# Kernel optimization log

Measured on AMD Instinct MI355X. Metric: run time of the kernel, lower is better.

The kernel has to match this reference:

```python
import jax, jax.numpy as jnp
import numpy as np

# Coarse-to-fine lossless 3D segmentation (Seg3dLossless), batch=1, C=1.
RES = [17, 33, 65, 129]          # odd resolutions, stride (RF-1)/(R-1) is integral
RF = RES[-1]
B_MIN, B_MAX = -1.0, 1.0
BAL = 0.5                        # balance_value
N_CONFLICT_ITERS = 2             # fixed unroll of the data-dependent while-loop


def _mlp(pts, w1, b1, w2, b2, w3, b3):
    # query_func: occupancy MLP on normalized (x,y,z) points -> [N]
    h = jax.nn.relu(pts @ w1 + b1)
    h = jax.nn.relu(h @ w2 + b2)
    return jax.nn.sigmoid(h @ w3 + b3)[..., 0]


def _eval_grid(R, w1, b1, w2, b2, w3, b3):
    # batch_eval with align_corners=False: coords2D = (coord + 0.5)/RF, mapped to [B_MIN,B_MAX]
    s = (RF - 1) // (R - 1)
    c = jnp.arange(R, dtype=jnp.float32) * s                 # final-res integer coords
    p = (c + 0.5) / RF * (B_MAX - B_MIN) + B_MIN
    zz, yy, xx = jnp.meshgrid(p, p, p, indexing='ij')        # [D,H,W]
    pts = jnp.stack([xx, yy, zz], axis=-1).reshape(-1, 3)    # (x,y,z) order
    return _mlp(pts, w1, b1, w2, b2, w3, b3).reshape(R, R, R)


def _resize(x, R):
    # trilinear, align_corners=True: out index j -> in coord j*(in-1)/(out-1)
    c = jnp.linspace(0.0, x.shape[0] - 1.0, R)
    zz, yy, xx = jnp.meshgrid(c, c, c, indexing='ij')
    return jax.scipy.ndimage.map_coordinates(x, [zz, yy, xx], order=1, mode='nearest')


def _dilate(m):
    # smooth_conv3x3 (mean filter) followed by >0 == 3x3x3 binary dilation
    f = jax.lax.reduce_window(m.astype(jnp.float32), 0.0, jax.lax.max,
                              (3, 3, 3), (1, 1, 1), 'SAME')
    return f > 0.0


def setup_inputs() -> dict:
    key = jax.random.key(0)
    k1, k2, k3 = jax.random.split(key, 3)
    H = 64
    return {
        'w1': jax.random.normal(k1, (3, H), jnp.float32) * 0.8,
        'b1': jnp.zeros((H,), jnp.float32),
        'w2': jax.random.normal(k2, (H, H), jnp.float32) * (1.0 / np.sqrt(H)),
        'b2': jnp.zeros((H,), jnp.float32),
        'w3': jax.random.normal(k3, (H, 1), jnp.float32) * (1.0 / np.sqrt(H)),
        'b3': jnp.zeros((1,), jnp.float32),
    }


def reference(w1, b1, w2, b2, w3, b3):
    params = (w1, b1, w2, b2, w3, b3)
    # level 0: dense eval on the coarse grid
    occ = _eval_grid(RES[0], *params)                        # [R0,R0,R0]
    s0 = (RF - 1) // (RES[0] - 1)
    calculated = jnp.zeros((RF, RF, RF), bool).at[::s0, ::s0, ::s0].set(True)

    for R in RES[1:]:
        s = (RF - 1) // (R - 1)
        valid = _resize((occ > BAL).astype(jnp.float32), R)  # no-grad mask path
        occ_i = _resize(occ, R)                              # differentiable interp
        boundary = _dilate((valid > 0.0) & (valid < 1.0))
        calc_l = calculated[::s, ::s, ::s]
        boundary = boundary & (~calc_l)                      # skip already-evaluated voxels
        occ_true = _eval_grid(R, *params)                    # query_func at this level
        occ = jnp.where(boundary, occ_true, occ_i)           # scatter of occupancys_topk
        calc_l = calc_l | boundary
        # conflict resolution: re-query 3^3 neighbors of sign-flip voxels
        conflict = boundary & ((occ_i - BAL) * (occ_true - BAL) < 0.0)
        for _ in range(N_CONFLICT_ITERS):
            nbr = _dilate(conflict) & (~calc_l)
            occ_prev = occ
            occ = jnp.where(nbr, occ_true, occ)
            calc_l = calc_l | nbr
            conflict = nbr & ((occ_prev - BAL) * (occ_true - BAL) < 0.0)
        calculated = calculated.at[::s, ::s, ::s].set(calc_l)

    return occ[None, None]                                   # (1, 1, D, H, W)
```

## Files before the change

kernel.cpp:

```cpp
#include <hip/hip_runtime.h>

#define HH 64

static __global__ void k_set_ones(unsigned char* __restrict__ p, int n){
  int i = blockIdx.x * blockDim.x + threadIdx.x;
  if (i < n) p[i] = 1;
}

static __global__ void k_eval_mlp(
    const float* __restrict__ w1, const float* __restrict__ b1,
    const float* __restrict__ w2, const float* __restrict__ b2,
    const float* __restrict__ w3, const float* __restrict__ b3,
    float* __restrict__ out, int R, int s)
{
  __shared__ float sw1[3*HH];
  __shared__ float sb1[HH];
  __shared__ float sw2t[HH*HH];
  __shared__ float sb2[HH];
  __shared__ float sw3[HH];
  __shared__ float sb3s[1];
  const int t = threadIdx.x;
  for (int idx = t; idx < HH*HH; idx += 256){
    int j = idx >> 6, i = idx & 63;
    sw2t[idx] = w2[i*HH + j];
  }
  if (t < 3*HH) sw1[t] = w1[t];
  if (t < HH){ sb1[t] = b1[t]; sb2[t] = b2[t]; sw3[t] = w3[t]; }
  if (t == 0) sb3s[0] = b3[0];
  __syncthreads();

  const unsigned int n = (unsigned int)R * (unsigned int)R * (unsigned int)R;
  const int lane = t & 63;
  const int half = lane >> 5;
  const int ibase = half * 32;
  const unsigned int gwave = (blockIdx.x * 256u + (unsigned int)t) >> 6;
  const unsigned int pid = gwave * 32u + (unsigned int)(lane & 31);
  if (pid >= n) return;

  const unsigned int c = pid % (unsigned int)R;
  const unsigned int r = pid / (unsigned int)R;
  const unsigned int b = r % (unsigned int)R;
  const unsigned int a = r / (unsigned int)R;
  const float inv129x2 = 2.0f / 129.0f;
  const float x = ((float)(c * (unsigned int)s) + 0.5f) * inv129x2 - 1.0f;
  const float y = ((float)(b * (unsigned int)s) + 0.5f) * inv129x2 - 1.0f;
  const float z = ((float)(a * (unsigned int)s) + 0.5f) * inv129x2 - 1.0f;

  float h1[32];
  #pragma unroll
  for (int k = 0; k < 32; ++k){
    int i = ibase + k;
    float v = sb1[i];
    v = fmaf(x, sw1[i],        v);
    v = fmaf(y, sw1[HH + i],   v);
    v = fmaf(z, sw1[2*HH + i], v);
    h1[k] = fmaxf(v, 0.0f);
  }
  float o = sb3s[0];
  #pragma unroll 4
  for (int j = 0; j < HH; ++j){
    const float* wr = &sw2t[j*HH + ibase];
    float acc = 0.0f;
    #pragma unroll
    for (int k = 0; k < 32; ++k) acc = fmaf(h1[k], wr[k], acc);
    acc += __shfl_xor(acc, 32);
    o = fmaf(fmaxf(acc + sb2[j], 0.0f), sw3[j], o);
  }
  if (half == 0) out[pid] = 1.0f / (1.0f + expf(-o));
}

static __global__ void k_eval_sparse(
    const float* __restrict__ w1, const float* __restrict__ b1,
    const float* __restrict__ w2, const float* __restrict__ b2,
    const float* __restrict__ w3, const float* __restrict__ b3,
    const int* __restrict__ idxl, const unsigned int* __restrict__ cnt,
    const float* __restrict__ occ_i,
    float* __restrict__ out, unsigned char* __restrict__ mism,
    int R, int s)
{
  if (blockIdx.x * 128u >= *cnt) return;
  __shared__ float sw1[3*HH];
  __shared__ float sb1[HH];
  __shared__ float sw2t[HH*HH];
  __shared__ float sb2[HH];
  __shared__ float sw3[HH];
  __shared__ float sb3s[1];
  const int t = threadIdx.x;
  for (int idx = t; idx < HH*HH; idx += 256){
    int j = idx >> 6, i = idx & 63;
    sw2t[idx] = w2[i*HH + j];
  }
  if (t < 3*HH) sw1[t] = w1[t];
  if (t < HH){ sb1[t] = b1[t]; sb2[t] = b2[t]; sw3[t] = w3[t]; }
  if (t == 0) sb3s[0] = b3[0];
  __syncthreads();

  const unsigned int count = *cnt;
  const int lane = t & 63;
  const int half = lane >> 5;
  const int ibase = half * 32;
  const unsigned int gwave = (blockIdx.x * 256u + (unsigned int)t) >> 6;
  const unsigned int slot = gwave * 32u + (unsigned int)(lane & 31);
  if (slot >= count) return;
  const unsigned int pid = (unsigned int)idxl[slot];

  const unsigned int c = pid % (unsigned int)R;
  const unsigned int r = pid / (unsigned int)R;
  const unsigned int b = r % (unsigned int)R;
  const unsigned int a = r / (unsigned int)R;
  const float inv129x2 = 2.0f / 129.0f;
  const float x = ((float)(c * (unsigned int)s) + 0.5f) * inv129x2 - 1.0f;
  const float y = ((float)(b * (unsigned int)s) + 0.5f) * inv129x2 - 1.0f;
  const float z = ((float)(a * (unsigned int)s) + 0.5f) * inv129x2 - 1.0f;

  float h1[32];
  #pragma unroll
  for (int k = 0; k < 32; ++k){
    int i = ibase + k;
    float v = sb1[i];
    v = fmaf(x, sw1[i],        v);
    v = fmaf(y, sw1[HH + i],   v);
    v = fmaf(z, sw1[2*HH + i], v);
    h1[k] = fmaxf(v, 0.0f);
  }
  float o = sb3s[0];
  #pragma unroll 4
  for (int j = 0; j < HH; ++j){
    const float* wr = &sw2t[j*HH + ibase];
    float acc = 0.0f;
    #pragma unroll
    for (int k = 0; k < 32; ++k) acc = fmaf(h1[k], wr[k], acc);
    acc += __shfl_xor(acc, 32);
    o = fmaf(fmaxf(acc + sb2[j], 0.0f), sw3[j], o);
  }
  if (half == 0){
    float ot = 1.0f / (1.0f + expf(-o));
    out[pid] = ot;
    mism[pid] = ((occ_i[pid] - 0.5f) * (ot - 0.5f) < 0.0f) ? (unsigned char)1 : (unsigned char)0;
  }
}

static __global__ __launch_bounds__(256) void k_resize_b0(
    const float* __restrict__ prev,
    const unsigned char* __restrict__ calc_prev,
    float* __restrict__ occ_i,
    unsigned char* __restrict__ bnd0,
    unsigned char* __restrict__ calc_out,
    int R, int Rp)
{
  const unsigned int n = (unsigned int)R * (unsigned int)R * (unsigned int)R;
  unsigned int gid = blockIdx.x * 256u + threadIdx.x;
  if (gid >= n) return;
  int c = (int)(gid % (unsigned int)R);
  unsigned int r = gid / (unsigned int)R;
  int b = (int)(r % (unsigned int)R);
  int a = (int)(r / (unsigned int)R);
  int a0 = a >> 1, da = a & 1;
  int b0i = b >> 1, db = b & 1;
  int c0 = c >> 1, dc = c & 1;
  float sum = 0.0f;
  int cnt = 0;
  const int tot = (da + 1) * (db + 1) * (dc + 1);
  for (int dz = 0; dz <= da; ++dz)
    for (int dy = 0; dy <= db; ++dy)
      for (int dx = 0; dx <= dc; ++dx){
        float v = prev[((unsigned int)(a0 + dz) * (unsigned int)Rp + (unsigned int)(b0i + dy)) * (unsigned int)Rp + (unsigned int)(c0 + dx)];
        sum += v;
        cnt += (v > 0.5f) ? 1 : 0;
      }
  occ_i[gid] = sum / (float)tot;
  bnd0[gid] = (cnt > 0 && cnt < tot) ? 1 : 0;
  calc_out[gid] = ((da | db | dc) == 0)
      ? calc_prev[((unsigned int)a0 * (unsigned int)Rp + (unsigned int)b0i) * (unsigned int)Rp + (unsigned int)c0]
      : (unsigned char)0;
}

static __global__ __launch_bounds__(256) void k_resize_boundary(
    const float* __restrict__ prev, const float* __restrict__ occ_true,
    const unsigned char* __restrict__ calc_prev,
    float* __restrict__ occ_i, unsigned char* __restrict__ bnd0,
    unsigned char* __restrict__ mism, unsigned char* __restrict__ calc_out,
    int R, int Rp)
{
  const unsigned int n = (unsigned int)R * (unsigned int)R * (unsigned int)R;
  unsigned int gid = blockIdx.x * 256u + threadIdx.x;
  if (gid >= n) return;
  int c = (int)(gid % (unsigned int)R);
  unsigned int r = gid / (unsigned int)R;
  int b = (int)(r % (unsigned int)R);
  int a = (int)(r / (unsigned int)R);
  int a0 = a >> 1, da = a & 1;
  int b0i = b >> 1, db = b & 1;
  int c0 = c >> 1, dc = c & 1;
  float sum = 0.0f;
  int cnt = 0;
  const int tot = (da + 1) * (db + 1) * (dc + 1);
  for (int dz = 0; dz <= da; ++dz)
    for (int dy = 0; dy <= db; ++dy)
      for (int dx = 0; dx <= dc; ++dx){
        float v = prev[((unsigned int)(a0 + dz) * (unsigned int)Rp + (unsigned int)(b0i + dy)) * (unsigned int)Rp + (unsigned int)(c0 + dx)];
        sum += v;
        cnt += (v > 0.5f) ? 1 : 0;
      }
  float oi = sum / (float)tot;
  occ_i[gid] = oi;
  bnd0[gid] = (cnt > 0 && cnt < tot) ? 1 : 0;
  mism[gid] = ((oi - 0.5f) * (occ_true[gid] - 0.5f) < 0.0f) ? 1 : 0;
  calc_out[gid] = ((da | db | dc) == 0)
      ? calc_prev[((unsigned int)a0 * (unsigned int)Rp + (unsigned int)b0i) * (unsigned int)Rp + (unsigned int)c0]
      : (unsigned char)0;
}

static __global__ void k_zero3(unsigned char* __restrict__ a, unsigned char* __restrict__ b,
                               unsigned char* __restrict__ c, unsigned int* __restrict__ cnt,
                               unsigned int nwords)
{
  unsigned int i = blockIdx.x * 256u + threadIdx.x;
  if (i == 0) *cnt = 0u;
  if (i < nwords){
    uint4 z = make_uint4(0u,0u,0u,0u);
    ((uint4*)a)[i] = z;
    ((uint4*)b)[i] = z;
    ((uint4*)c)[i] = z;
  }
}

static __global__ __launch_bounds__(256) void k_dil7(
    const unsigned char* __restrict__ in, unsigned char* __restrict__ outp,
    int R, int axis)
{
  const unsigned int n = (unsigned int)R * (unsigned int)R * (unsigned int)R;
  unsigned int gid = blockIdx.x * 256u + threadIdx.x;
  if (gid >= n) return;
  int c = (int)(gid % (unsigned int)R);
  unsigned int r = gid / (unsigned int)R;
  int b = (int)(r % (unsigned int)R);
  int a = (int)(r / (unsigned int)R);
  int coord = (axis == 0) ? c : ((axis == 1) ? b : a);
  int stride = (axis == 0) ? 1 : ((axis == 1) ? R : R * R);
  int g = (int)gid;
  int m = 0;
  #pragma unroll
  for (int d = -3; d <= 3; ++d){
    int q = coord + d;
    if (q >= 0 && q < R) m |= in[g + d * stride];
  }
  outp[gid] = (unsigned char)(m ? 1 : 0);
}

static __global__ __launch_bounds__(256) void k_count(
    const unsigned char* __restrict__ cand, unsigned int* __restrict__ bcnt,
    unsigned int n)
{
  unsigned int gid = blockIdx.x * 256u + threadIdx.x;
  bool pred = (gid < n) && (cand[gid] != 0);
  unsigned long long m = __ballot(pred);
  __shared__ unsigned int wc[4];
  int wid = (int)(threadIdx.x >> 6);
  if ((threadIdx.x & 63u) == 0) wc[wid] = (unsigned int)__popcll(m);
  __syncthreads();
  if (threadIdx.x == 0) bcnt[blockIdx.x] = wc[0] + wc[1] + wc[2] + wc[3];
}

static __global__ __launch_bounds__(1024) void k_scan(
    unsigned int* __restrict__ bcnt, unsigned int nb, unsigned int* __restrict__ total)
{
  __shared__ unsigned int part[1024];
  const unsigned int t = threadIdx.x;
  const unsigned int chunk = (nb + 1023u) / 1024u;
  const unsigned int beg = t * chunk;
  const unsigned int end = (beg + chunk < nb) ? (beg + chunk) : nb;
  unsigned int s = 0;
  for (unsigned int i = beg; i < end; ++i) s += bcnt[i];
  part[t] = s;
  __syncthreads();
  for (int offd = 1; offd < 1024; offd <<= 1){
    unsigned int v = (t >= (unsigned int)offd) ? part[t - offd] : 0u;
    __syncthreads();
    part[t] += v;
    __syncthreads();
  }
  unsigned int run = (t == 0) ? 0u : part[t - 1];
  for (unsigned int i = beg; i < end; ++i){
    unsigned int v = bcnt[i];
    bcnt[i] = run;
    run += v;
  }
  if (t == 1023) *total = part[1023];
}

static __global__ __launch_bounds__(256) void k_scatter(
    const unsigned char* __restrict__ cand, const unsigned int* __restrict__ boff,
    int* __restrict__ idxl, unsigned int n)
{
  unsigned int gid = blockIdx.x * 256u + threadIdx.x;
  bool pred = (gid < n) && (cand[gid] != 0);
  unsigned long long m = __ballot(pred);
  __shared__ unsigned int wbase[4];
  int wid = (int)(threadIdx.x >> 6);
  int lane = (int)(threadIdx.x & 63u);
  if (lane == 0) wbase[wid] = (unsigned int)__popcll(m);
  __syncthreads();
  if (threadIdx.x == 0){
    unsigned int b = boff[blockIdx.x];
    unsigned int t0 = wbase[0], t1 = wbase[1], t2 = wbase[2];
    wbase[0] = b; wbase[1] = b + t0; wbase[2] = b + t0 + t1; wbase[3] = b + t0 + t1 + t2;
  }
  __syncthreads();
  if (pred){
    int pre = __popcll(m & ((1ull << lane) - 1ull));
    idxl[wbase[wid] + (unsigned int)pre] = (int)gid;
  }
}

static __global__ __launch_bounds__(256) void k_dilate_sparse(
    const int* __restrict__ idxl, const unsigned int* __restrict__ cnt,
    const unsigned char* __restrict__ src, const unsigned char* __restrict__ mism,
    unsigned char* __restrict__ calc, unsigned char* __restrict__ conf_out,
    unsigned char* __restrict__ upd, int R)
{
  const unsigned int count = *cnt;
  for (unsigned int slot = blockIdx.x * 256u + threadIdx.x; slot < count;
       slot += gridDim.x * 256u){
    int gid = idxl[slot];
    int c = gid % R;
    int r = gid / R;
    int b = r % R;
    int a = r / R;
    int m = 0;
    for (int dz = -1; dz <= 1; ++dz){
      int az = a + dz; if (az < 0 || az >= R) continue;
      for (int dy = -1; dy <= 1; ++dy){
        int by = b + dy; if (by < 0 || by >= R) continue;
        for (int dx = -1; dx <= 1; ++dx){
          int cx = c + dx; if (cx < 0 || cx >= R) continue;
          m |= src[(az * R + by) * R + cx];
        }
      }
    }
    unsigned char nb = (m && !calc[gid]) ? (unsigned char)1 : (unsigned char)0;
    conf_out[gid] = (nb && mism[gid]) ? (unsigned char)1 : (unsigned char)0;
    if (nb){ calc[gid] = 1; upd[gid] = 1; }
  }
}

static __global__ __launch_bounds__(256) void k_dilate_step(
    const unsigned char* __restrict__ src, const unsigned char* __restrict__ mism,
    unsigned char* __restrict__ calc, unsigned char* __restrict__ conf_out,
    unsigned char* __restrict__ upd, int R, int first)
{
  const unsigned int n = (unsigned int)R * (unsigned int)R * (unsigned int)R;
  unsigned int gid = blockIdx.x * 256u + threadIdx.x;
  if (gid >= n) return;
  int c = (int)(gid % (unsigned int)R);
  unsigned int r = gid / (unsigned int)R;
  int b = (int)(r % (unsigned int)R);
  int a = (int)(r / (unsigned int)R);
  int m = 0;
  for (int dz = -1; dz <= 1; ++dz){
    int az = a + dz; if (az < 0 || az >= R) continue;
    for (int dy = -1; dy <= 1; ++dy){
      int by = b + dy; if (by < 0 || by >= R) continue;
      for (int dx = -1; dx <= 1; ++dx){
        int cx = c + dx; if (cx < 0 || cx >= R) continue;
        m |= src[((unsigned int)az * (unsigned int)R + (unsigned int)by) * (unsigned int)R + (unsigned int)cx];
      }
    }
  }
  unsigned char nb = (m && !calc[gid]) ? (unsigned char)1 : (unsigned char)0;
  if (nb) calc[gid] = 1;
  conf_out[gid] = (nb && mism[gid]) ? (unsigned char)1 : (unsigned char)0;
  if (first) upd[gid] = nb;
  else if (nb) upd[gid] = 1;
}

static __global__ __launch_bounds__(256) void k_combine(
    const float* __restrict__ occ_true, const float* __restrict__ occ_i,
    const unsigned char* __restrict__ upd, float* __restrict__ out, unsigned int n)
{
  unsigned int gid = blockIdx.x * 256u + threadIdx.x;
  if (gid < n) out[gid] = upd[gid] ? occ_true[gid] : occ_i[gid];
}

extern "C" void kernel_launch(void* const* d_in, const int* in_sizes, int n_in,
                              void* d_out, int out_size, void* d_ws, size_t ws_size,
                              hipStream_t stream)
{
  const float* w1 = (const float*)d_in[0];
  const float* b1 = (const float*)d_in[1];
  const float* w2 = (const float*)d_in[2];
  const float* b2 = (const float*)d_in[3];
  const float* w3 = (const float*)d_in[4];
  const float* b3 = (const float*)d_in[5];
  float* out = (float*)d_out;

  const int NF = 129 * 129 * 129;
  const int NP = 65 * 65 * 65;
  char* ws = (char*)d_ws;
  size_t off = 0;
  auto alloc = [&](size_t bytes) -> void* {
    void* p = (void*)(ws + off);
    off += (bytes + 255) & ~(size_t)255;
    return p;
  };
  float* f_true  = (float*)alloc((size_t)NF * 4);
  float* f_occi  = (float*)alloc((size_t)NF * 4);
  float* f_prevA = (float*)alloc((size_t)NP * 4);
  float* f_prevB = (float*)alloc((size_t)NP * 4);
  int*   i_idx   = (int*)alloc((size_t)NF * 4);
  unsigned int* u_cnt  = (unsigned int*)alloc(256);
  unsigned int* u_bcnt = (unsigned int*)alloc(8448 * 4);
  unsigned char* b_b0    = (unsigned char*)alloc(NF);
  unsigned char* b_mism  = (unsigned char*)alloc(NF);
  unsigned char* b_confA = (unsigned char*)alloc(NF);
  unsigned char* b_confB = (unsigned char*)alloc(NF);
  unsigned char* b_calcA = (unsigned char*)alloc(NF);
  unsigned char* b_calcB = (unsigned char*)alloc(NF);
  unsigned char* b_upd   = (unsigned char*)alloc(NF);
  unsigned char* b_cand  = (unsigned char*)alloc(NF);
  unsigned char* b_tmp   = (unsigned char*)alloc(NF);
  (void)ws_size;

  auto eval_blocks = [](int n){ return (n + 127) / 128; };

  {
    int R = 17, s = 8;
    int n = R * R * R;
    k_eval_mlp<<<eval_blocks(n), 256, 0, stream>>>(w1, b1, w2, b2, w3, b3, f_prevA, R, s);
    k_set_ones<<<(n + 255) / 256, 256, 0, stream>>>(b_calcA, n);
  }

  int Rp = 17;
  float* prev = f_prevA;
  unsigned char* calcP = b_calcA;
  unsigned char* calcC = b_calcB;
  for (int li = 1; li <= 3; ++li){
    int R = 2 * Rp - 1;
    int s = 128 / (R - 1);
    unsigned int n = (unsigned int)R * (unsigned int)R * (unsigned int)R;
    int blocks = (int)((n + 255u) / 256u);
    float* occ_out = (li == 3) ? out : ((prev == f_prevA) ? f_prevB : f_prevA);

    if (R == 33){
      k_eval_mlp<<<eval_blocks((int)n), 256, 0, stream>>>(w1, b1, w2, b2, w3, b3, f_true, R, s);
      k_resize_boundary<<<blocks, 256, 0, stream>>>(prev, f_true, calcP, f_occi, b_b0, b_mism, calcC, R, Rp);
      k_dilate_step<<<blocks, 256, 0, stream>>>(b_b0,    b_mism, calcC, b_confA, b_upd, R, 1);
      k_dilate_step<<<blocks, 256, 0, stream>>>(b_confA, b_mism, calcC, b_confB, b_upd, R, 0);
      k_dilate_step<<<blocks, 256, 0, stream>>>(b_confB, b_mism, calcC, b_confA, b_upd, R, 0);
      k_combine<<<blocks, 256, 0, stream>>>(f_true, f_occi, b_upd, occ_out, n);
    } else {
      unsigned int nwords = (n + 15u) / 16u;
      int zblocks = (int)((nwords + 255u) / 256u);
      k_resize_b0<<<blocks, 256, 0, stream>>>(prev, calcP, f_occi, b_b0, calcC, R, Rp);
      k_zero3<<<zblocks, 256, 0, stream>>>(b_confA, b_confB, b_upd, u_cnt, nwords);
      k_dil7<<<blocks, 256, 0, stream>>>(b_b0,   b_cand, R, 0);
      k_dil7<<<blocks, 256, 0, stream>>>(b_cand, b_tmp,  R, 1);
      k_dil7<<<blocks, 256, 0, stream>>>(b_tmp,  b_cand, R, 2);
      k_count<<<blocks, 256, 0, stream>>>(b_cand, u_bcnt, n);
      k_scan<<<1, 1024, 0, stream>>>(u_bcnt, (unsigned int)blocks, u_cnt);
      k_scatter<<<blocks, 256, 0, stream>>>(b_cand, u_bcnt, i_idx, n);
      k_eval_sparse<<<eval_blocks((int)n), 256, 0, stream>>>(
          w1, b1, w2, b2, w3, b3, i_idx, u_cnt, f_occi, f_true, b_mism, R, s);
      int sblocks = blocks < 4096 ? blocks : 4096;
      k_dilate_sparse<<<sblocks, 256, 0, stream>>>(i_idx, u_cnt, b_b0,    b_mism, calcC, b_confA, b_upd, R);
      k_dilate_sparse<<<sblocks, 256, 0, stream>>>(i_idx, u_cnt, b_confA, b_mism, calcC, b_confB, b_upd, R);
      k_dilate_sparse<<<sblocks, 256, 0, stream>>>(i_idx, u_cnt, b_confB, b_mism, calcC, b_confA, b_upd, R);
      k_combine<<<blocks, 256, 0, stream>>>(f_true, f_occi, b_upd, occ_out, n);
    }

    prev = occ_out;
    unsigned char* tmpc = calcP; calcP = calcC; calcC = tmpc;
    Rp = R;
  }
  (void)in_sizes; (void)n_in; (void)out_size;
}
```

Baseline: 332.0 us.

## Fuse combine into dilation, merge zeroing and y/z dilation passes, persistent sparse eval

Pre-transposes w2 once so each MLP block copies it into shared memory with vectorized loads instead of a strided transpose. The zeroing kernel is folded into resize, and the y/z separable dilations are merged with the block count. The final combine pass is replaced by writing the interpolated value in resize and overwriting updated voxels during the last sparse dilation step. The sparse eval uses a capped grid-stride loop so blocks load weights once and process several chunks. Together these cut kernel launches and full-grid passes, at the cost of a 7x7 yz window per voxel and more scattered writes in the sparse kernels.

Result: slower. 340.1 us (+2.5%).

```diff
diff --git a/kernel.cpp b/kernel.cpp
--- a/kernel.cpp
+++ b/kernel.cpp
@@ -7,9 +7,14 @@
   if (i < n) p[i] = 1;
 }
 
+static __global__ void k_prep_w2t(const float* __restrict__ w2, float* __restrict__ w2t){
+  int t = blockIdx.x * 256 + threadIdx.x;
+  w2t[t] = w2[(t & 63) * HH + (t >> 6)];
+}
+
 static __global__ void k_eval_mlp(
     const float* __restrict__ w1, const float* __restrict__ b1,
-    const float* __restrict__ w2, const float* __restrict__ b2,
+    const float* __restrict__ w2t, const float* __restrict__ b2,
     const float* __restrict__ w3, const float* __restrict__ b3,
     float* __restrict__ out, int R, int s)
 {
@@ -20,9 +25,10 @@
   __shared__ float sw3[HH];
   __shared__ float sb3s[1];
   const int t = threadIdx.x;
-  for (int idx = t; idx < HH*HH; idx += 256){
-    int j = idx >> 6, i = idx & 63;
-    sw2t[idx] = w2[i*HH + j];
+  {
+    const float4* src4 = (const float4*)w2t;
+    float4* dst4 = (float4*)sw2t;
+    for (int idx = t; idx < HH*HH/4; idx += 256) dst4[idx] = src4[idx];
   }
   if (t < 3*HH) sw1[t] = w1[t];
   if (t < HH){ sb1[t] = b1[t]; sb2[t] = b2[t]; sw3[t] = w3[t]; }
@@ -71,14 +77,16 @@
 
 static __global__ void k_eval_sparse(
     const float* __restrict__ w1, const float* __restrict__ b1,
-    const float* __restrict__ w2, const float* __restrict__ b2,
+    const float* __restrict__ w2t, const float* __restrict__ b2,
     const float* __restrict__ w3, const float* __restrict__ b3,
     const int* __restrict__ idxl, const unsigned int* __restrict__ cnt,
     const float* __restrict__ occ_i,
     float* __restrict__ out, unsigned char* __restrict__ mism,
     int R, int s)
 {
-  if (blockIdx.x * 128u >= *cnt) return;
+  const unsigned int count = *cnt;
+  const unsigned int chunks = (count + 127u) >> 7;
+  if (blockIdx.x >= chunks) return;
   __shared__ float sw1[3*HH];
   __shared__ float sb1[HH];
   __shared__ float sw2t[HH*HH];
@@ -86,57 +94,60 @@
   __shared__ float sw3[HH];
   __shared__ float sb3s[1];
   const int t = threadIdx.x;
-  for (int idx = t; idx < HH*HH; idx += 256){
-    int j = idx >> 6, i = idx & 63;
-    sw2t[idx] = w2[i*HH + j];
+  {
+    const float4* src4 = (const float4*)w2t;
+    float4* dst4 = (float4*)sw2t;
+    for (int idx = t; idx < HH*HH/4; idx += 256) dst4[idx] = src4[idx];
   }
   if (t < 3*HH) sw1[t] = w1[t];
   if (t < HH){ sb1[t] = b1[t]; sb2[t] = b2[t]; sw3[t] = w3[t]; }
   if (t == 0) sb3s[0] = b3[0];
   __syncthreads();
 
-  const unsigned int count = *cnt;
   const int lane = t & 63;
   const int half = lane >> 5;
   const int ibase = half * 32;
-  const unsigned int gwave = (blockIdx.x * 256u + (unsigned int)t) >> 6;
-  const unsigned int slot = gwave * 32u + (unsigned int)(lane & 31);
-  if (slot >= count) return;
-  const unsigned int pid = (unsigned int)idxl[slot];
-
-  const unsigned int c = pid % (unsigned int)R;
-  const unsigned int r = pid / (unsigned int)R;
-  const unsigned int b = r % (unsigned int)R;
-  const unsigned int a = r / (unsigned int)R;
+  const int wid = t >> 6;
   const float inv129x2 = 2.0f / 129.0f;
-  const float x = ((float)(c * (unsigned int)s) + 0.5f) * inv129x2 - 1.0f;
-  const float y = ((float)(b * (unsigned int)s) + 0.5f) * inv129x2 - 1.0f;
-  const float z = ((float)(a * (unsigned int)s) + 0.5f) * inv129x2 - 1.0f;
-
-  float h1[32];
-  #pragma unroll
-  for (int k = 0; k < 32; ++k){
-    int i = ibase + k;
-    float v = sb1[i];
-    v = fmaf(x, sw1[i],        v);
-    v = fmaf(y, sw1[HH + i],   v);
-    v = fmaf(z, sw1[2*HH + i], v);
-    h1[k] = fmaxf(v, 0.0f);
-  }
-  float o = sb3s[0];
-  #pragma unroll 4
-  for (int j = 0; j < HH; ++j){
-    const float* wr = &sw2t[j*HH + ibase];
-    float acc = 0.0f;
+
+  for (unsigned int chunk = blockIdx.x; chunk < chunks; chunk += gridDim.x){
+    const unsigned int slot = chunk * 128u + (unsigned int)(wid * 32 + (lane & 31));
+    if (slot >= count) continue;
+    const unsigned int pid = (unsigned int)idxl[slot];
+
+    const unsigned int c = pid % (unsigned int)R;
+    const unsigned int r = pid / (unsigned int)R;
+    const unsigned int b = r % (unsigned int)R;
+    const unsigned int a = r / (unsigned int)R;
+    const float x = ((float)(c * (unsigned int)s) + 0.5f) * inv129x2 - 1.0f;
+    const float y = ((float)(b * (unsigned int)s) + 0.5f) * inv129x2 - 1.0f;
+    const float z = ((float)(a * (unsigned int)s) + 0.5f) * inv129x2 - 1.0f;
+
+    float h1[32];
     #pragma unroll
-    for (int k = 0; k < 32; ++k) acc = fmaf(h1[k], wr[k], acc);
-    acc += __shfl_xor(acc, 32);
-    o = fmaf(fmaxf(acc + sb2[j], 0.0f), sw3[j], o);
-  }
-  if (half == 0){
-    float ot = 1.0f / (1.0f + expf(-o));
-    out[pid] = ot;
-    mism[pid] = ((occ_i[pid] - 0.5f) * (ot - 0.5f) < 0.0f) ? (unsigned char)1 : (unsigned char)0;
+    for (int k = 0; k < 32; ++k){
+      int i = ibase + k;
+      float v = sb1[i];
+      v = fmaf(x, sw1[i],        v);
+      v = fmaf(y, sw1[HH + i],   v);
+      v = fmaf(z, sw1[2*HH + i], v);
+      h1[k] = fmaxf(v, 0.0f);
+    }
+    float o = sb3s[0];
+    #pragma unroll 4
+    for (int j = 0; j < HH; ++j){
+      const float* wr = &sw2t[j*HH + ibase];
+      float acc = 0.0f;
+      #pragma unroll
+      for (int k = 0; k < 32; ++k) acc = fmaf(h1[k], wr[k], acc);
+      acc += __shfl_xor(acc, 32);
+      o = fmaf(fmaxf(acc + sb2[j], 0.0f), sw3[j], o);
+    }
+    if (half == 0){
+      float ot = 1.0f / (1.0f + expf(-o));
+      out[pid] = ot;
+      mism[pid] = ((occ_i[pid] - 0.5f) * (ot - 0.5f) < 0.0f) ? (unsigned char)1 : (unsigned char)0;
+    }
   }
 }
 
@@ -144,42 +155,12 @@
     const float* __restrict__ prev,
     const unsigned char* __restrict__ calc_prev,
     float* __restrict__ occ_i,
+    float* __restrict__ occ_out,
     unsigned char* __restrict__ bnd0,
     unsigned char* __restrict__ calc_out,
-    int R, int Rp)
-{
-  const unsigned int n = (unsigned int)R * (unsigned int)R * (unsigned int)R;
-  unsigned int gid = blockIdx.x * 256u + threadIdx.x;
-  if (gid >= n) return;
-  int c = (int)(gid % (unsigned int)R);
-  unsigned int r = gid / (unsigned int)R;
-  int b = (int)(r % (unsigned int)R);
-  int a = (int)(r / (unsigned int)R);
-  int a0 = a >> 1, da = a & 1;
-  int b0i = b >> 1, db = b & 1;
-  int c0 = c >> 1, dc = c & 1;
-  float sum = 0.0f;
-  int cnt = 0;
-  const int tot = (da + 1) * (db + 1) * (dc + 1);
-  for (int dz = 0; dz <= da; ++dz)
-    for (int dy = 0; dy <= db; ++dy)
-      for (int dx = 0; dx <= dc; ++dx){
-        float v = prev[((unsigned int)(a0 + dz) * (unsigned int)Rp + (unsigned int)(b0i + dy)) * (unsigned int)Rp + (unsigned int)(c0 + dx)];
-        sum += v;
-        cnt += (v > 0.5f) ? 1 : 0;
-      }
-  occ_i[gid] = sum / (float)tot;
-  bnd0[gid] = (cnt > 0 && cnt < tot) ? 1 : 0;
-  calc_out[gid] = ((da | db | dc) == 0)
-      ? calc_prev[((unsigned int)a0 * (unsigned int)Rp + (unsigned int)b0i) * (unsigned int)Rp + (unsigned int)c0]
-      : (unsigned char)0;
-}
-
-static __global__ __launch_bounds__(256) void k_resize_boundary(
-    const float* __restrict__ prev, const float* __restrict__ occ_true,
-    const unsigned char* __restrict__ calc_prev,
-    float* __restrict__ occ_i, unsigned char* __restrict__ bnd0,
-    unsigned char* __restrict__ mism, unsigned char* __restrict__ calc_out,
+    unsigned char* __restrict__ confA,
+    unsigned char* __restrict__ confB,
+    unsigned char* __restrict__ upd,
     int R, int Rp)
 {
   const unsigned int n = (unsigned int)R * (unsigned int)R * (unsigned int)R;
@@ -204,6 +185,45 @@
       }
   float oi = sum / (float)tot;
   occ_i[gid] = oi;
+  occ_out[gid] = oi;
+  bnd0[gid] = (cnt > 0 && cnt < tot) ? 1 : 0;
+  calc_out[gid] = ((da | db | dc) == 0)
+      ? calc_prev[((unsigned int)a0 * (unsigned int)Rp + (unsigned int)b0i) * (unsigned int)Rp + (unsigned int)c0]
+      : (unsigned char)0;
+  confA[gid] = 0; confB[gid] = 0; upd[gid] = 0;
+}
+
+static __global__ __launch_bounds__(256) void k_resize_boundary(
+    const float* __restrict__ prev, const float* __restrict__ occ_true,
+    const unsigned char* __restrict__ calc_prev,
+    float* __restrict__ occ_i, float* __restrict__ occ_out,
+    unsigned char* __restrict__ bnd0,
+    unsigned char* __restrict__ mism, unsigned char* __restrict__ calc_out,
+    int R, int Rp)
+{
+  const unsigned int n = (unsigned int)R * (unsigned int)R * (unsigned int)R;
+  unsigned int gid = blockIdx.x * 256u + threadIdx.x;
+  if (gid >= n) return;
+  int c = (int)(gid % (unsigned int)R);
+  unsigned int r = gid / (unsigned int)R;
+  int b = (int)(r % (unsigned int)R);
+  int a = (int)(r / (unsigned int)R);
+  int a0 = a >> 1, da = a & 1;
+  int b0i = b >> 1, db = b & 1;
+  int c0 = c >> 1, dc = c & 1;
+  float sum = 0.0f;
+  int cnt = 0;
+  const int tot = (da + 1) * (db + 1) * (dc + 1);
+  for (int dz = 0; dz <= da; ++dz)
+    for (int dy = 0; dy <= db; ++dy)
+      for (int dx = 0; dx <= dc; ++dx){
+        float v = prev[((unsigned int)(a0 + dz) * (unsigned int)Rp + (unsigned int)(b0i + dy)) * (unsigned int)Rp + (unsigned int)(c0 + dx)];
+        sum += v;
+        cnt += (v > 0.5f) ? 1 : 0;
+      }
+  float oi = sum / (float)tot;
+  occ_i[gid] = oi;
+  occ_out[gid] = oi;
   bnd0[gid] = (cnt > 0 && cnt < tot) ? 1 : 0;
   mism[gid] = ((oi - 0.5f) * (occ_true[gid] - 0.5f) < 0.0f) ? 1 : 0;
   calc_out[gid] = ((da | db | dc) == 0)
@@ -211,53 +231,50 @@
       : (unsigned char)0;
 }
 
-static __global__ void k_zero3(unsigned char* __restrict__ a, unsigned char* __restrict__ b,
-                               unsigned char* __restrict__ c, unsigned int* __restrict__ cnt,
-                               unsigned int nwords)
-{
-  unsigned int i = blockIdx.x * 256u + threadIdx.x;
-  if (i == 0) *cnt = 0u;
-  if (i < nwords){
-    uint4 z = make_uint4(0u,0u,0u,0u);
-    ((uint4*)a)[i] = z;
-    ((uint4*)b)[i] = z;
-    ((uint4*)c)[i] = z;
-  }
-}
-
-static __global__ __launch_bounds__(256) void k_dil7(
-    const unsigned char* __restrict__ in, unsigned char* __restrict__ outp,
-    int R, int axis)
+static __global__ __launch_bounds__(256) void k_dil7x(
+    const unsigned char* __restrict__ in, unsigned char* __restrict__ outp, int R)
 {
   const unsigned int n = (unsigned int)R * (unsigned int)R * (unsigned int)R;
   unsigned int gid = blockIdx.x * 256u + threadIdx.x;
   if (gid >= n) return;
   int c = (int)(gid % (unsigned int)R);
-  unsigned int r = gid / (unsigned int)R;
-  int b = (int)(r % (unsigned int)R);
-  int a = (int)(r / (unsigned int)R);
-  int coord = (axis == 0) ? c : ((axis == 1) ? b : a);
-  int stride = (axis == 0) ? 1 : ((axis == 1) ? R : R * R);
   int g = (int)gid;
   int m = 0;
   #pragma unroll
   for (int d = -3; d <= 3; ++d){
-    int q = coord + d;
-    if (q >= 0 && q < R) m |= in[g + d * stride];
+    int q = c + d;
+    if (q >= 0 && q < R) m |= in[g + d];
   }
   outp[gid] = (unsigned char)(m ? 1 : 0);
 }
 
-static __global__ __launch_bounds__(256) void k_count(
-    const unsigned char* __restrict__ cand, unsigned int* __restrict__ bcnt,
-    unsigned int n)
-{
-  unsigned int gid = blockIdx.x * 256u + threadIdx.x;
-  bool pred = (gid < n) && (cand[gid] != 0);
-  unsigned long long m = __ballot(pred);
+static __global__ __launch_bounds__(256) void k_dil7yz_count(
+    const unsigned char* __restrict__ in, unsigned char* __restrict__ outp,
+    unsigned int* __restrict__ bcnt, int R)
+{
+  const unsigned int n = (unsigned int)R * (unsigned int)R * (unsigned int)R;
+  unsigned int gid = blockIdx.x * 256u + threadIdx.x;
+  int m = 0;
+  if (gid < n){
+    int c = (int)(gid % (unsigned int)R);
+    unsigned int r = gid / (unsigned int)R;
+    int b = (int)(r % (unsigned int)R);
+    int a = (int)(r / (unsigned int)R);
+    int base = (int)gid;
+    for (int dz = -3; dz <= 3; ++dz){
+      int az = a + dz; if (az < 0 || az >= R) continue;
+      for (int dy = -3; dy <= 3; ++dy){
+        int by = b + dy; if (by < 0 || by >= R) continue;
+        m |= in[base + dz * R * R + dy * R];
+      }
+    }
+    outp[gid] = (unsigned char)(m ? 1 : 0);
+    (void)c;
+  }
+  unsigned long long bm = __ballot(m != 0);
   __shared__ unsigned int wc[4];
   int wid = (int)(threadIdx.x >> 6);
-  if ((threadIdx.x & 63u) == 0) wc[wid] = (unsigned int)__popcll(m);
+  if ((threadIdx.x & 63u) == 0) wc[wid] = (unsigned int)__popcll(bm);
   __syncthreads();
   if (threadIdx.x == 0) bcnt[blockIdx.x] = wc[0] + wc[1] + wc[2] + wc[3];
 }
@@ -317,7 +334,8 @@
     const int* __restrict__ idxl, const unsigned int* __restrict__ cnt,
     const unsigned char* __restrict__ src, const unsigned char* __restrict__ mism,
     unsigned char* __restrict__ calc, unsigned char* __restrict__ conf_out,
-    unsigned char* __restrict__ upd, int R)
+    unsigned char* __restrict__ upd, int R, int final_step,
+    const float* __restrict__ occ_true, float* __restrict__ occ_out)
 {
   const unsigned int count = *cnt;
   for (unsigned int slot = blockIdx.x * 256u + threadIdx.x; slot < count;
@@ -340,14 +358,17 @@
     }
     unsigned char nb = (m && !calc[gid]) ? (unsigned char)1 : (unsigned char)0;
     conf_out[gid] = (nb && mism[gid]) ? (unsigned char)1 : (unsigned char)0;
-    if (nb){ calc[gid] = 1; upd[gid] = 1; }
+    unsigned char u = upd[gid];
+    if (nb){ calc[gid] = 1; if (!u){ upd[gid] = 1; u = 1; } }
+    if (final_step && u) occ_out[gid] = occ_true[gid];
   }
 }
 
 static __global__ __launch_bounds__(256) void k_dilate_step(
     const unsigned char* __restrict__ src, const unsigned char* __restrict__ mism,
     unsigned char* __restrict__ calc, unsigned char* __restrict__ conf_out,
-    unsigned char* __restrict__ upd, int R, int first)
+    unsigned char* __restrict__ upd, int R, int first, int final_step,
+    const float* __restrict__ occ_true, float* __restrict__ occ_out)
 {
   const unsigned int n = (unsigned int)R * (unsigned int)R * (unsigned int)R;
   unsigned int gid = blockIdx.x * 256u + threadIdx.x;
@@ -370,16 +391,10 @@
   unsigned char nb = (m && !calc[gid]) ? (unsigned char)1 : (unsigned char)0;
   if (nb) calc[gid] = 1;
   conf_out[gid] = (nb && mism[gid]) ? (unsigned char)1 : (unsigned char)0;
-  if (first) upd[gid] = nb;
-  else if (nb) upd[gid] = 1;
-}
-
-static __global__ __launch_bounds__(256) void k_combine(
-    const float* __restrict__ occ_true, const float* __restrict__ occ_i,
-    const unsigned char* __restrict__ upd, float* __restrict__ out, unsigned int n)
-{
-  unsigned int gid = blockIdx.x * 256u + threadIdx.x;
-  if (gid < n) out[gid] = upd[gid] ? occ_true[gid] : occ_i[gid];
+  unsigned char u;
+  if (first){ u = nb; upd[gid] = nb; }
+  else { u = upd[gid]; if (nb && !u){ upd[gid] = 1; u = 1; } }
+  if (final_step && u) occ_out[gid] = occ_true[gid];
 }
 
 extern "C" void kernel_launch(void* const* d_in, const int* in_sizes, int n_in,
@@ -407,6 +422,7 @@
   float* f_occi  = (float*)alloc((size_t)NF * 4);
   float* f_prevA = (float*)alloc((size_t)NP * 4);
   float* f_prevB = (float*)alloc((size_t)NP * 4);
+  float* f_w2t   = (float*)alloc((size_t)HH * HH * 4);
   int*   i_idx   = (int*)alloc((size_t)NF * 4);
   unsigned int* u_cnt  = (unsigned int*)alloc(256);
   unsigned int* u_bcnt = (unsigned int*)alloc(8448 * 4);
@@ -423,10 +439,12 @@
 
   auto eval_blocks = [](int n){ return (n + 127) / 128; };
 
+  k_prep_w2t<<<16, 256, 0, stream>>>(w2, f_w2t);
+
   {
     int R = 17, s = 8;
     int n = R * R * R;
-    k_eval_mlp<<<eval_blocks(n), 256, 0, stream>>>(w1, b1, w2, b2, w3, b3, f_prevA, R, s);
+    k_eval_mlp<<<eval_blocks(n), 256, 0, stream>>>(w1, b1, f_w2t, b2, w3, b3, f_prevA, R, s);
     k_set_ones<<<(n + 255) / 256, 256, 0, stream>>>(b_calcA, n);
   }
 
@@ -442,30 +460,25 @@
     float* occ_out = (li == 3) ? out : ((prev == f_prevA) ? f_prevB : f_prevA);
 
     if (R == 33){
-      k_eval_mlp<<<eval_blocks((int)n), 256, 0, stream>>>(w1, b1, w2, b2, w3, b3, f_true, R, s);
-      k_resize_boundary<<<blocks, 256, 0, stream>>>(prev, f_true, calcP, f_occi, b_b0, b_mism, calcC, R, Rp);
-      k_dilate_step<<<blocks, 256, 0, stream>>>(b_b0,    b_mism, calcC, b_confA, b_upd, R, 1);
-      k_dilate_step<<<blocks, 256, 0, stream>>>(b_confA, b_mism, calcC, b_confB, b_upd, R, 0);
-      k_dilate_step<<<blocks, 256, 0, stream>>>(b_confB, b_mism, calcC, b_confA, b_upd, R, 0);
-      k_combine<<<blocks, 256, 0, stream>>>(f_true, f_occi, b_upd, occ_out, n);
+      k_eval_mlp<<<eval_blocks((int)n), 256, 0, stream>>>(w1, b1, f_w2t, b2, w3, b3, f_true, R, s);
+      k_resize_boundary<<<blocks, 256, 0, stream>>>(prev, f_true, calcP, f_occi, occ_out, b_b0, b_mism, calcC, R, Rp);
+      k_dilate_step<<<blocks, 256, 0, stream>>>(b_b0,    b_mism, calcC, b_confA, b_upd, R, 1, 0, f_true, occ_out);
+      k_dilate_step<<<blocks, 256, 0, stream>>>(b_confA, b_mism, calcC, b_confB, b_upd, R, 0, 0, f_true, occ_out);
+      k_dilate_step<<<blocks, 256, 0, stream>>>(b_confB, b_mism, calcC, b_confA, b_upd, R, 0, 1, f_true, occ_out);
     } else {
-      unsigned int nwords = (n + 15u) / 16u;
-      int zblocks = (int)((nwords + 255u) / 256u);
-      k_resize_b0<<<blocks, 256, 0, stream>>>(prev, calcP, f_occi, b_b0, calcC, R, Rp);
-      k_zero3<<<zblocks, 256, 0, stream>>>(b_confA, b_confB, b_upd, u_cnt, nwords);
-      k_dil7<<<blocks, 256, 0, stream>>>(b_b0,   b_cand, R, 0);
-      k_dil7<<<blocks, 256, 0, stream>>>(b_cand, b_tmp,  R, 1);
-      k_dil7<<<blocks, 256, 0, stream>>>(b_tmp,  b_cand, R, 2);
-      k_count<<<blocks, 256, 0, stream>>>(b_cand, u_bcnt, n);
+      k_resize_b0<<<blocks, 256, 0, stream>>>(prev, calcP, f_occi, occ_out, b_b0, calcC,
+                                              b_confA, b_confB, b_upd, R, Rp);
+      k_dil7x<<<blocks, 256, 0, stream>>>(b_b0, b_tmp, R);
+      k_dil7yz_count<<<blocks, 256, 0, stream>>>(b_tmp, b_cand, u_bcnt, R);
       k_scan<<<1, 1024, 0, stream>>>(u_bcnt, (unsigned int)blocks, u_cnt);
       k_scatter<<<blocks, 256, 0, stream>>>(b_cand, u_bcnt, i_idx, n);
-      k_eval_sparse<<<eval_blocks((int)n), 256, 0, stream>>>(
-          w1, b1, w2, b2, w3, b3, i_idx, u_cnt, f_occi, f_true, b_mism, R, s);
+      int egrid = eval_blocks((int)n); if (egrid > 2048) egrid = 2048;
+      k_eval_sparse<<<egrid, 256, 0, stream>>>(
+          w1, b1, f_w2t, b2, w3, b3, i_idx, u_cnt, f_occi, f_true, b_mism, R, s);
       int sblocks = blocks < 4096 ? blocks : 4096;
-      k_dilate_sparse<<<sblocks, 256, 0, stream>>>(i_idx, u_cnt, b_b0,    b_mism, calcC, b_confA, b_upd, R);
-      k_dilate_sparse<<<sblocks, 256, 0, stream>>>(i_idx, u_cnt, b_confA, b_mism, calcC, b_confB, b_upd, R);
-      k_dilate_sparse<<<sblocks, 256, 0, stream>>>(i_idx, u_cnt, b_confB, b_mism, calcC, b_confA, b_upd, R);
-      k_combine<<<blocks, 256, 0, stream>>>(f_true, f_occi, b_upd, occ_out, n);
+      k_dilate_sparse<<<sblocks, 256, 0, stream>>>(i_idx, u_cnt, b_b0,    b_mism, calcC, b_confA, b_upd, R, 0, f_true, occ_out);
+      k_dilate_sparse<<<sblocks, 256, 0, stream>>>(i_idx, u_cnt, b_confA, b_mism, calcC, b_confB, b_upd, R, 0, f_true, occ_out);
+      k_dilate_sparse<<<sblocks, 256, 0, stream>>>(i_idx, u_cnt, b_confB, b_mism, calcC, b_confA, b_upd, R, 1, f_true, occ_out);
     }
 
     prev = occ_out;
```
